# Kernel optimization log

Measured on AMD Instinct MI355X. Metric: run time of the kernel, lower is better.

The kernel has to match this reference:

```python
import jax, jax.numpy as jnp
import numpy as np

N_CLASSES = 16384
M = 2
D = 128


def setup_inputs() -> dict:
    key = jax.random.key(0)
    k1, k2 = jax.random.split(key)
    x = jax.random.normal(k1, (N_CLASSES * M, D), dtype=jnp.float32)
    anchor_idx = jax.random.randint(k2, (N_CLASSES,), 0, M, dtype=jnp.int64 if jax.config.jax_enable_x64 else jnp.int32).astype(jnp.int32)
    pos_idx = (1 - anchor_idx).astype(jnp.int32)  # randperm(2) -> positive is the other sample
    return {"x": x, "anchor_idx": anchor_idx, "pos_idx": pos_idx}


def reference(x, anchor_idx, pos_idx):
    # x: [N*M, D]; anchor_idx/pos_idx: [N] in [0, M)
    N = anchor_idx.shape[0]
    Dx = x.shape[1]
    xr = x.reshape(N, M, Dx)
    anchors = jnp.take_along_axis(xr, anchor_idx[:, None, None], axis=1)[:, 0, :]    # [N, D]
    positives = jnp.take_along_axis(xr, pos_idx[:, None, None], axis=1)[:, 0, :]     # [N, D]
    negs = xr[:, 1, :]                                                               # [N, D] (sample 1 of every class)
    # score[i, j] = a_i . (neg_j - pos_i) = a_i . neg_j - a_i . pos_i
    S = anchors @ negs.T                                                             # [N, N]
    ap = jnp.sum(anchors * positives, axis=1)                                        # [N]
    logits = S - ap[:, None]
    mask = ~jnp.eye(N, dtype=bool)                                                   # exclude j == i (own class)
    sums = jnp.sum(jnp.where(mask, jnp.exp(logits), jnp.float32(0.0)), axis=1)       # [N]
    return jnp.sum(jnp.log1p(sums))
```

## Files before the change

kernel.cpp:

```cpp
#include <hip/hip_runtime.h>
#include <hip/hip_bf16.h>
#include <math.h>

#define N_CLS 16384
#define DDIM  128
#define CSHIFT 50.0f
#define LOG2E 1.4426950408889634f
#define NEGC2 (-72.13475204444817f)

#if __has_builtin(__builtin_amdgcn_exp2f)
#define EXP2(x) __builtin_amdgcn_exp2f(x)
#else
#define EXP2(x) exp2f(x)
#endif

typedef __attribute__((ext_vector_type(8))) short short8;
typedef __attribute__((ext_vector_type(4))) float f32x4;

__device__ __forceinline__ unsigned short f2bf(float f) {
    __hip_bfloat16 h = __float2bfloat16(f);
    return *(unsigned short*)&h;
}

__global__ __launch_bounds__(256)
void prep_kernel(const float* __restrict__ x,
                 const int* __restrict__ aidx,
                 float* __restrict__ ap,
                 unsigned short* __restrict__ Afrag,
                 unsigned short* __restrict__ Bfrag,
                 float* __restrict__ out) {
    const int t = threadIdx.x;
    const int tl = blockIdx.x;
    const int kc = t >> 6, q = (t >> 4) & 3, m = t & 15;
    const int col = kc * 32 + q * 8;
    const int i = tl * 16 + m;

    float fa[8], fb[8];
    *(float4*)&fa[0] = *(const float4*)(x + (2L * i) * DDIM + col);
    *(float4*)&fa[4] = *(const float4*)(x + (2L * i) * DDIM + col + 4);
    *(float4*)&fb[0] = *(const float4*)(x + (2L * i + 1) * DDIM + col);
    *(float4*)&fb[4] = *(const float4*)(x + (2L * i + 1) * DDIM + col + 4);
    const bool sel = (aidx[i] != 0);

    short8 As8, Bs8;
    float d = 0.0f;
    #pragma unroll
    for (int j = 0; j < 8; ++j) {
        const float av = sel ? fb[j] : fa[j];
        As8[j] = (short)f2bf(av * LOG2E);
        Bs8[j] = (short)f2bf(fb[j]);
        d += fa[j] * fb[j];
    }
    *(short8*)(Afrag + (long)tl * 2048 + t * 8) = As8;
    *(short8*)(Bfrag + (long)tl * 2048 + t * 8) = Bs8;

    d += __shfl_xor(d, 16, 64);
    d += __shfl_xor(d, 32, 64);
    __shared__ float sap[4][16];
    if ((t & 63) < 16) sap[kc][t & 63] = d;
    __syncthreads();
    if (t < 16) ap[tl * 16 + t] = sap[0][t] + sap[1][t] + sap[2][t] + sap[3][t];
    if (t == 0 && tl == 0) out[0] = 0.0f;
}

__global__ __launch_bounds__(256, 2)
void fused_kernel(const unsigned short* __restrict__ Afrag,
                  const unsigned short* __restrict__ Bfrag,
                  float* __restrict__ partial) {
    const int tid = threadIdx.x;
    const int lane = tid & 63;
    const int w = tid >> 6;
    const int quad = lane >> 4;
    const int l15 = lane & 15;
    const int oct = blockIdx.x & 7;
    const int rt = blockIdx.x >> 3;
    const int wm2 = w >> 1;
    const int wh = w & 1;

    short8 af[4][4];
    {
        const unsigned short* abase =
            Afrag + ((long)(rt * 8 + wm2 * 4) * 4) * 512 + lane * 8;
        #pragma unroll
        for (int mt = 0; mt < 4; ++mt)
            #pragma unroll
            for (int kc = 0; kc < 4; ++kc)
                af[mt][kc] = *(const short8*)(abase + (mt * 4 + kc) * 512);
    }

    const unsigned short* bbase =
        Bfrag + ((long)(oct * 128 + wh * 4) * 4) * 512 + lane * 8;

    const f32x4 cinit = (f32x4){NEGC2, NEGC2, NEGC2, NEGC2};
    float rs[4][4] = {};
    short8 bP[4], bQ[4];
    f32x4 accA[4], accB[4];

    const bool canDiag = ((rt >> 4) == oct) && (wm2 == wh);
    const int itd = canDiag ? (rt & 15) : -1;

    auto stage = [&](f32x4 (&aC)[4], f32x4 (&aO)[4],
                     short8 (&bC)[4], short8 (&bN)[4],
                     const unsigned short* nxt, int mtd, bool doEpi) {
        #pragma unroll
        for (int g = 0; g < 4; ++g) {
            bN[g] = *(const short8*)(nxt + g * 512);
            if (g == 0) {
                #pragma unroll
                for (int mt = 0; mt < 4; ++mt)
                    aC[mt] = __builtin_amdgcn_mfma_f32_16x16x32_bf16(
                        af[mt][0], bC[0], cinit, 0, 0, 0);
            } else {
                #pragma unroll
                for (int mt = 0; mt < 4; ++mt)
                    aC[mt] = __builtin_amdgcn_mfma_f32_16x16x32_bf16(
                        af[mt][g], bC[g], aC[mt], 0, 0, 0);
            }
            if (doEpi) {
                #pragma unroll
                for (int reg = 0; reg < 4; ++reg) {
                    float e = EXP2(aO[g][reg]);
                    if (g == mtd && quad * 4 + reg == l15) e = 0.0f;
                    rs[g][reg] += e;
                }
            }
        }
    };

    #pragma unroll
    for (int kc = 0; kc < 4; ++kc)
        bP[kc] = *(const short8*)(bbase + kc * 512);

    bool dprev = false;
    for (int it = 0; it < 16; ++it) {
        const unsigned short* p1 = bbase + (long)it * 16384;
        const bool d = (it == itd);
        stage(accA, accB, bP, bQ, p1 + 2048, dprev ? 3 : -1, it > 0);
        stage(accB, accA, bQ, bP, p1 + 4096, d ? 0 : -1, true);
        stage(accA, accB, bP, bQ, p1 + 6144, d ? 1 : -1, true);
        const unsigned short* p2 = bbase + (long)((it < 15) ? it + 1 : it) * 16384;
        stage(accB, accA, bQ, bP, p2, d ? 2 : -1, true);
        dprev = d;
    }
    #pragma unroll
    for (int mt = 0; mt < 4; ++mt)
        #pragma unroll
        for (int reg = 0; reg < 4; ++reg) {
            float e = EXP2(accB[mt][reg]);
            if (dprev && mt == 3 && quad * 4 + reg == l15) e = 0.0f;
            rs[mt][reg] += e;
        }

    const int slot = oct * 2 + wh;
    const int rowBase = rt * 128 + wm2 * 64;
    #pragma unroll
    for (int mt = 0; mt < 4; ++mt)
        #pragma unroll
        for (int reg = 0; reg < 4; ++reg) {
            float v = rs[mt][reg];
            v += __shfl_xor(v, 1, 64);
            v += __shfl_xor(v, 2, 64);
            v += __shfl_xor(v, 4, 64);
            v += __shfl_xor(v, 8, 64);
            if (l15 == 0)
                partial[(long)slot * N_CLS + rowBase + mt * 16 + quad * 4 + reg] = v;
        }
}

__global__ __launch_bounds__(256)
void finalize_kernel(const float* __restrict__ partial,
                     const float* __restrict__ ap,
                     float* __restrict__ out) {
    __shared__ float red[256];
    const int t = threadIdx.x;
    const int row = blockIdx.x * 256 + t;
    float s = 0.0f;
    #pragma unroll
    for (int p = 0; p < 16; ++p) s += partial[(long)p * N_CLS + row];
    const float u = logf(s) + (CSHIFT - ap[row]);
    const float loss = (u > 25.0f) ? u : log1pf(__expf(u));
    red[t] = loss;
    __syncthreads();
    for (int st = 128; st > 0; st >>= 1) {
        if (t < st) red[t] += red[t + st];
        __syncthreads();
    }
    if (t == 0) atomicAdd(out, red[0]);
}

extern "C" void kernel_launch(void* const* d_in, const int* in_sizes, int n_in,
                              void* d_out, int out_size, void* d_ws, size_t ws_size,
                              hipStream_t stream) {
    const float* x    = (const float*)d_in[0];
    const int*   aidx = (const int*)d_in[1];

    char* ws = (char*)d_ws;
    float* ap             = (float*)(ws);
    float* partial        = (float*)(ws + 131072);
    unsigned short* Afrag = (unsigned short*)(ws + 131072 + 1048576);
    unsigned short* Bfrag = (unsigned short*)(ws + 131072 + 1048576 + 4194304);

    prep_kernel<<<N_CLS / 16, 256, 0, stream>>>(x, aidx, ap, Afrag, Bfrag, (float*)d_out);
    fused_kernel<<<1024, 256, 0, stream>>>(Afrag, Bfrag, partial);
    finalize_kernel<<<64, 256, 0, stream>>>(partial, ap, (float*)d_out);
}
```

Measured before the change: 133.7 us.

## Stage B fragments through double-buffered LDS via global_load_lds

```diff
diff --git a/kernel.cpp b/kernel.cpp
--- a/kernel.cpp
+++ b/kernel.cpp
@@ -16,6 +16,8 @@
 
 typedef __attribute__((ext_vector_type(8))) short short8;
 typedef __attribute__((ext_vector_type(4))) float f32x4;
+typedef const __attribute__((address_space(1))) void* gas_t;
+typedef __attribute__((address_space(3))) void* las_t;
 
 __device__ __forceinline__ unsigned short f2bf(float f) {
     __hip_bfloat16 h = __float2bfloat16(f);
@@ -67,6 +69,8 @@
 void fused_kernel(const unsigned short* __restrict__ Afrag,
                   const unsigned short* __restrict__ Bfrag,
                   float* __restrict__ partial) {
+    __shared__ unsigned short Bs[2][16384];
+
     const int tid = threadIdx.x;
     const int lane = tid & 63;
     const int w = tid >> 6;
@@ -77,6 +81,16 @@
     const int wm2 = w >> 1;
     const int wh = w & 1;
 
+    auto stage_load = [&](int it2, int p2) {
+        const unsigned short* g = Bfrag + (long)oct * 262144 + (long)it2 * 16384
+                                + w * 4096 + lane * 8;
+        #pragma unroll
+        for (int j = 0; j < 8; ++j)
+            __builtin_amdgcn_global_load_lds(
+                (gas_t)(g + j * 512),
+                (las_t)(&Bs[p2][w * 4096 + j * 512]), 16, 0, 0);
+    };
+
     short8 af[4][4];
     {
         const unsigned short* abase =
@@ -88,9 +102,6 @@
                 af[mt][kc] = *(const short8*)(abase + (mt * 4 + kc) * 512);
     }
 
-    const unsigned short* bbase =
-        Bfrag + ((long)(oct * 128 + wh * 4) * 4) * 512 + lane * 8;
-
     const f32x4 cinit = (f32x4){NEGC2, NEGC2, NEGC2, NEGC2};
     float rs[4][4] = {};
     short8 bP[4], bQ[4];
@@ -104,7 +115,7 @@
                      const unsigned short* nxt, int mtd, bool doEpi) {
         #pragma unroll
         for (int g = 0; g < 4; ++g) {
-            bN[g] = *(const short8*)(nxt + g * 512);
+            if (nxt) bN[g] = *(const short8*)(nxt + g * 512);
             if (g == 0) {
                 #pragma unroll
                 for (int mt = 0; mt < 4; ++mt)
@@ -127,19 +138,34 @@
         }
     };
 
-    #pragma unroll
-    for (int kc = 0; kc < 4; ++kc)
-        bP[kc] = *(const short8*)(bbase + kc * 512);
+    stage_load(0, 0);
+    __syncthreads();
+    {
+        const unsigned short* B0 = &Bs[0][wh * 8192 + lane * 8];
+        #pragma unroll
+        for (int kc = 0; kc < 4; ++kc)
+            bP[kc] = *(const short8*)(B0 + kc * 512);
+    }
 
     bool dprev = false;
     for (int it = 0; it < 16; ++it) {
-        const unsigned short* p1 = bbase + (long)it * 16384;
+        const int p = it & 1;
+        if (it < 15) stage_load(it + 1, p ^ 1);
+
+        const unsigned short* Bp = &Bs[p][wh * 8192 + lane * 8];
         const bool d = (it == itd);
-        stage(accA, accB, bP, bQ, p1 + 2048, dprev ? 3 : -1, it > 0);
-        stage(accB, accA, bQ, bP, p1 + 4096, d ? 0 : -1, true);
-        stage(accA, accB, bP, bQ, p1 + 6144, d ? 1 : -1, true);
-        const unsigned short* p2 = bbase + (long)((it < 15) ? it + 1 : it) * 16384;
-        stage(accB, accA, bQ, bP, p2, d ? 2 : -1, true);
+        stage(accA, accB, bP, bQ, Bp + 2048, dprev ? 3 : -1, it > 0);
+        stage(accB, accA, bQ, bP, Bp + 4096, d ? 0 : -1, true);
+        stage(accA, accB, bP, bQ, Bp + 6144, d ? 1 : -1, true);
+        stage(accB, accA, bQ, bP, nullptr, d ? 2 : -1, true);
+
+        __syncthreads();
+        if (it < 15) {
+            const unsigned short* Bn = &Bs[p ^ 1][wh * 8192 + lane * 8];
+            #pragma unroll
+            for (int kc = 0; kc < 4; ++kc)
+                bP[kc] = *(const short8*)(Bn + kc * 512);
+        }
         dprev = d;
     }
     #pragma unroll
```

Result: no change. 135.4 us (+1.3%).
